# Optimization experiments

Measured on AMD Instinct MI355X. Metric: run time of the kernel, lower is better.

Reference implementation:

```python
import jax, jax.numpy as jnp
import numpy as np

N = 20000      # nodes
E = 640000     # edges
R = 90         # relations
IN_F = 128     # raw feature dim
HID = 64       # hidden_channels
OUT = 32       # out_channels of conv2
NCLASS = 4
NB = 35        # num_bases (conv1)
EPS = 1e-16    # PyG softmax epsilon


def setup_inputs() -> dict:
    key = jax.random.key(0)
    ks = jax.random.split(key, 16)
    s = 0.1
    return {
        "x": jax.random.normal(ks[0], (N, IN_F), jnp.float32),
        "edge_index": jax.random.randint(ks[1], (2, E), 0, N, jnp.int32),
        "edge_type": jax.random.randint(ks[2], (E,), 0, R, jnp.int32),
        "edge_attr": jax.random.normal(ks[3], (E, 16), jnp.float32),
        # lin1: in_channels -> hidden (no bias)
        "lin1_w": jax.random.normal(ks[4], (IN_F, HID), jnp.float32) * s,
        # conv1: basis decomposition, heads=2, out=20, dim=2 -> H*O=40, H*dim=4
        "att1": jax.random.normal(ks[5], (R, NB), jnp.float32) * s,
        "basis1": jax.random.normal(ks[6], (NB, HID, 40), jnp.float32) * s,
        "q1": jax.random.normal(ks[7], (40, 4), jnp.float32) * s,
        "k1": jax.random.normal(ks[8], (40, 4), jnp.float32) * s,
        "wmod1": jnp.ones((20,), jnp.float32),            # mod='additive' weight (init ones)
        "bias1": jnp.zeros((80,), jnp.float32),            # concat bias: H*dim*O = 80
        # conv2: block-diagonal, in=80, blocks=2, H*O=64, H*dim=2
        "w2": jax.random.normal(ks[9], (R, 2, 40, 32), jnp.float32) * s,
        "q2": jax.random.normal(ks[10], (64, 2), jnp.float32) * s,
        "k2": jax.random.normal(ks[11], (64, 2), jnp.float32) * s,
        "lin_edge_w": jax.random.normal(ks[12], (16, 64), jnp.float32) * s,
        "e2": jax.random.normal(ks[13], (64, 2), jnp.float32) * s,
        # lin2: 2*out -> nclass
        "lin2_w": jax.random.normal(ks[14], (2 * OUT, NCLASS), jnp.float32) * s,
        "lin2_b": jnp.zeros((NCLASS,), jnp.float32),
    }


def segment_softmax(alpha, seg, num_segments):
    # PyG softmax: exp(x - detach(segment_max)) / (segment_sum + 1e-16)
    m = jax.ops.segment_max(alpha, seg, num_segments=num_segments)
    e = jnp.exp(alpha - jax.lax.stop_gradient(m)[seg])
    ssum = jax.ops.segment_sum(e, seg, num_segments=num_segments)
    return e / (ssum[seg] + EPS)


def rgat_forward(x, edge_index, edge_type, edge_attr, lin1_w, att1, basis1,
                 q1, k1, wmod1, bias1, w2, q2, k2, lin_edge_w, e2, lin2_w, lin2_b):
    src, dst = edge_index[0], edge_index[1]   # x_j = x[src], x_i = x[dst]
    n = x.shape[0]
    e = src.shape[0]

    h = x @ lin1_w                            # [N, HID]

    # ---- conv1: basis decomposition, within-relation, multiplicative attn, mod='additive'
    w = jnp.einsum('rb,bio->rio', att1, basis1)          # [R, HID, 40]
    xw = jnp.einsum('ni,rio->rno', h, w)                 # [R, N, 40] (all-relation transform)
    outj = xw[edge_type, src]                            # [E, 40]
    outi = xw[edge_type, dst]                            # [E, 40]
    qi = outi @ q1                                       # [E, 4]
    kj = outj @ k1                                       # [E, 4]
    alpha = qi * kj                                      # multiplicative-self-attention
    seg = dst.astype(jnp.int32) * R + edge_type          # within-relation softmax groups
    alpha = segment_softmax(alpha, seg, n * R)           # [E, 4]
    outj4 = outj.reshape(e, 2, 1, 20)                    # [E, H, 1, O]
    hmod = wmod1 * jnp.broadcast_to(outj4, (e, 2, 2, 20))  # mod='additive' term
    msg = outj4 * alpha.reshape(e, 2, 2, 1) + hmod       # [E, H, dim, O]
    agg = jax.ops.segment_sum(msg, dst, num_segments=n)  # [N, 2, 2, 20]
    h1 = agg.reshape(n, 80) + bias1
    h1 = jax.nn.relu(h1)

    # ---- conv2: block-diagonal, across-relation, additive attn, edge features, no bias
    xb = h1.reshape(n, 2, 40)
    xw2 = jnp.einsum('nbc,rbcd->rnbd', xb, w2).reshape(R, n, 64)  # [R, N, 64]
    outj = xw2[edge_type, src]                           # [E, 64]
    outi = xw2[edge_type, dst]
    qi = outi @ q2                                       # [E, 2]
    kj = outj @ k2
    ae = (edge_attr @ lin_edge_w) @ e2                   # [E, 2]
    alpha = jax.nn.leaky_relu(qi + kj + ae, 0.2)         # additive-self-attention
    alpha = segment_softmax(alpha, dst, n)               # across-relation
    msg = alpha.reshape(e, 2, 1) * outj.reshape(e, 2, 32)
    h2 = jax.ops.segment_sum(msg, dst, num_segments=n).reshape(n, 64)

    out = h2 @ lin2_w + lin2_b
    return jax.nn.log_softmax(out, axis=-1)


def reference(x, edge_index, edge_type, edge_attr, lin1_w, att1, basis1, q1, k1,
              wmod1, bias1, w2, q2, k2, lin_edge_w, e2, lin2_w, lin2_b):
    return rgat_forward(x, edge_index, edge_type, edge_attr, lin1_w, att1, basis1,
                        q1, k1, wmod1, bias1, w2, q2, k2, lin_edge_w, e2, lin2_w, lin2_b)
```

## Files before the change

kernel.cpp:

```cpp
#include <hip/hip_runtime.h>
#include <math.h>

constexpr int NN   = 20000;
constexpr int EE   = 640000;
constexpr int RR   = 90;
constexpr int INF_ = 128;
constexpr int HID  = 64;
constexpr float EPS = 1e-16f;
constexpr int E2   = 646144;

typedef unsigned short u16;
typedef _Float16 f16;
typedef __attribute__((ext_vector_type(8))) _Float16 f16x8;
typedef __attribute__((ext_vector_type(4))) _Float16 f16x4;
typedef __attribute__((ext_vector_type(4))) float f32x4;
typedef __attribute__((ext_vector_type(4))) int ivec4;

__device__ inline unsigned f2ord(float f) {
    unsigned u = __float_as_uint(f);
    return (u & 0x80000000u) ? ~u : (u | 0x80000000u);
}
__device__ inline float ord2f(unsigned x) {
    unsigned u = (x & 0x80000000u) ? (x & 0x7FFFFFFFu) : ~x;
    return __uint_as_float(u);
}
#define ORD_NEGINF 0x007FFFFFu

__global__ void k_fillrec(int4* p, int n) {
    int i = blockIdx.x * blockDim.x + threadIdx.x;
    if (i < n) { int4 r; r.x = 0; r.y = 0; r.z = 0; r.w = -1; p[i] = r; }
}

__global__ void k_hist(const int* et, int* hist) {
    __shared__ int lh[RR];
    if (threadIdx.x < RR) lh[threadIdx.x] = 0;
    __syncthreads();
    int i = blockIdx.x * blockDim.x + threadIdx.x;
    if (i < EE) atomicAdd(&lh[et[i]], 1);
    __syncthreads();
    if (threadIdx.x < RR) atomicAdd(&hist[threadIdx.x], lh[threadIdx.x]);
}

__global__ void k_scanPad(const int* hist, int* cursor) {
    if (threadIdx.x == 0) {
        int acc = 0;
        for (int r = 0; r < RR; ++r) {
            cursor[r] = acc;
            acc += (hist[r] + 63) & ~63;
        }
    }
}

__global__ void k_scatter(const int* src, const int* dst, const int* et,
                          int* cursor, int4* sortedR, int* posS) {
    __shared__ int lh[RR];
    __shared__ int lbase[RR];
    if (threadIdx.x < RR) lh[threadIdx.x] = 0;
    __syncthreads();
    int i = blockIdx.x * blockDim.x + threadIdx.x;
    int r = et[i];
    int rank = atomicAdd(&lh[r], 1);
    __syncthreads();
    if (threadIdx.x < RR) {
        int c = lh[threadIdx.x];
        lbase[threadIdx.x] = c ? atomicAdd(&cursor[threadIdx.x], c) : 0;
    }
    __syncthreads();
    int pos = lbase[r] + rank;
    int4 rec; rec.x = src[i]; rec.y = dst[i]; rec.z = r; rec.w = i;
    sortedR[pos] = rec;
    posS[i] = pos;
}

__global__ void k_histD(const int* dst, int* histD) {
    int i = blockIdx.x * blockDim.x + threadIdx.x;
    if (i < EE) atomicAdd(&histD[dst[i]], 1);
}

__global__ void k_scanD(const int* histD, int* rowptrD, int* cursorD) {
    __shared__ int part[256];
    const int CH = (NN + 255) / 256;
    int tid = threadIdx.x;
    int base = tid * CH;
    int s = 0;
    for (int j = 0; j < CH; ++j) {
        int idx = base + j;
        if (idx < NN) s += histD[idx];
    }
    part[tid] = s;
    __syncthreads();
    if (tid == 0) {
        int acc = 0;
        for (int t = 0; t < 256; ++t) { int v = part[t]; part[t] = acc; acc += v; }
    }
    __syncthreads();
    int acc = part[tid];
    for (int j = 0; j < CH; ++j) {
        int idx = base + j;
        if (idx < NN) {
            rowptrD[idx] = acc;
            cursorD[idx] = acc;
            acc += histD[idx];
        }
    }
    if (tid == 0) rowptrD[NN] = EE;
}

__global__ void k_scatterD(int4* sortedR, int* cursorD, u16* relD) {
    int i = blockIdx.x * blockDim.x + threadIdx.x;
    if (i >= E2) return;
    int4 rec = sortedR[i];
    if (rec.w < 0) return;
    int pos = atomicAdd(&cursorD[rec.y], 1);
    ((int*)(sortedR + i))[3] = pos;
    relD[pos] = (u16)rec.z;
}

__global__ void k_w1(const float* att1, const float* basis1, float* w1) {
    int idx = blockIdx.x * blockDim.x + threadIdx.x;
    if (idx >= RR * 2560) return;
    int r = idx / 2560, co = idx - r * 2560;
    float acc = 0.f;
    for (int b = 0; b < 35; ++b) acc += att1[r * 35 + b] * basis1[b * 2560 + co];
    w1[idx] = acc;
}

__global__ void k_wqk1(const float* w1, const float* q1, const float* k1,
                       float* wq1, float* wk1) {
    int idx = blockIdx.x * blockDim.x + threadIdx.x;
    if (idx >= RR * 64 * 4) return;
    int t = idx & 3, c = (idx >> 2) & 63, r = idx >> 8;
    const float* wrow = w1 + (size_t)r * 2560 + c * 40;
    float aq = 0.f, ak = 0.f;
    for (int o = 0; o < 40; ++o) {
        float w = wrow[o];
        aq += w * q1[o * 4 + t];
        ak += w * k1[o * 4 + t];
    }
    wq1[idx] = aq; wk1[idx] = ak;
}

__global__ void k_wqk2(const float* w2, const float* q2, const float* k2,
                       float* wq2, float* wk2) {
    int idx = blockIdx.x * blockDim.x + threadIdx.x;
    if (idx >= RR * 80 * 2) return;
    int t = idx & 1, bc = (idx >> 1) % 80, r = idx / 160;
    int b = bc / 40, c = bc % 40;
    const float* wbase = w2 + (size_t)((r * 2 + b) * 40 + c) * 32;
    float aq = 0.f, ak = 0.f;
    for (int d = 0; d < 32; ++d) {
        float w = wbase[d];
        aq += w * q2[(b * 32 + d) * 2 + t];
        ak += w * k2[(b * 32 + d) * 2 + t];
    }
    wq2[idx] = aq; wk2[idx] = ak;
}

__global__ void k_we(const float* lew, const float* e2, float* we) {
    int idx = threadIdx.x;
    if (idx >= 32) return;
    int i = idx >> 1, t = idx & 1;
    float acc = 0.f;
    for (int j = 0; j < 64; ++j) acc += lew[i * 64 + j] * e2[j * 2 + t];
    we[idx] = acc;
}

__global__ __launch_bounds__(256) void k_ae(const float* ea, const float* weg,
                                            const int* posS, float* aeS) {
    __shared__ float wes[32];
    if (threadIdx.x < 32) wes[threadIdx.x] = weg[threadIdx.x];
    __syncthreads();
    int e = blockIdx.x * 256 + threadIdx.x;
    if (e >= EE) return;
    const float4* ep = (const float4*)(ea + (size_t)e * 16);
    float a0 = 0.f, a1 = 0.f;
#pragma unroll
    for (int cc = 0; cc < 4; ++cc) {
        float4 v = ep[cc];
        const float* vv = (const float*)&v;
#pragma unroll
        for (int j = 0; j < 4; ++j) {
            int ii = cc * 4 + j;
            a0 = fmaf(vv[j], wes[ii * 2 + 0], a0);
            a1 = fmaf(vv[j], wes[ii * 2 + 1], a1);
        }
    }
    float2 av; av.x = a0; av.y = a1;
    *(float2*)(aeS + (size_t)posS[e] * 2) = av;
}

__global__ void k_w1hT(const float* w1, f16* w1hT) {
    int idx = blockIdx.x * blockDim.x + threadIdx.x;
    if (idx >= RR * 48 * 64) return;
    int k = idx & 63, o = (idx >> 6) % 48, r = idx / (48 * 64);
    float v = (o < 40) ? w1[(size_t)r * 2560 + k * 40 + o] : 0.f;
    w1hT[idx] = (f16)v;
}

__global__ void k_w2hT(const float* w2, f16* w2hT) {
    int idx = blockIdx.x * blockDim.x + threadIdx.x;
    if (idx >= RR * 2 * 32 * 64) return;
    int c = idx & 63, d = (idx >> 6) & 31, b = (idx >> 11) & 1, r = idx >> 12;
    float v = (c < 40) ? w2[((((size_t)r * 2 + b) * 40) + c) * 32 + d] : 0.f;
    w2hT[idx] = (f16)v;
}

__global__ void k_h(const float* x, const float* lin1_w, f16* hh) {
    __shared__ float xs[INF_];
    int n = blockIdx.x, t = threadIdx.x;
    xs[t]      = x[(size_t)n * INF_ + t];
    xs[t + 64] = x[(size_t)n * INF_ + t + 64];
    __syncthreads();
    float acc = 0.f;
    for (int i = 0; i < INF_; ++i) acc += xs[i] * lin1_w[i * HID + t];
    hh[(size_t)n * HID + t] = (f16)acc;
}

__global__ __launch_bounds__(256) void k_c1(const int4* sortedR, const f16* hh,
                                            const f16* w1hT,
                                            const float* wq1g, const float* wk1g,
                                            float* alpha1s, f16* outj1h) {
    __shared__ float qs[256], ks[256];
    int base = blockIdx.x * 64;
    int r = sortedR[base].z;
    qs[threadIdx.x] = wq1g[(size_t)r * 256 + threadIdx.x];
    ks[threadIdx.x] = wk1g[(size_t)r * 256 + threadIdx.x];
    __syncthreads();
    int wid = threadIdx.x >> 6, l = threadIdx.x & 63;
    int e0 = base + wid * 16;
    int row16 = l & 15, g = l >> 4;
    f16x8 a[3][2];
#pragma unroll
    for (int mt = 0; mt < 3; ++mt)
#pragma unroll
        for (int kk = 0; kk < 2; ++kk)
            a[mt][kk] = *(const f16x8*)(w1hT + ((size_t)r * 48 + mt * 16 + row16) * 64 + kk * 32 + g * 8);
    ivec4 er = __builtin_nontemporal_load((const ivec4*)(sortedR + e0 + row16));
    int s = er[0], d = er[1], pd = er[3];
    f16x8 b0 = *(const f16x8*)(hh + (size_t)s * 64 + g * 8);
    f16x8 b1 = *(const f16x8*)(hh + (size_t)s * 64 + 32 + g * 8);
    f16x8 d0 = *(const f16x8*)(hh + (size_t)d * 64 + g * 8);
    f16x8 d1 = *(const f16x8*)(hh + (size_t)d * 64 + 32 + g * 8);
    float qi[4] = {0.f, 0.f, 0.f, 0.f}, kj[4] = {0.f, 0.f, 0.f, 0.f};
#pragma unroll
    for (int j = 0; j < 8; ++j) {
        int p0 = g * 8 + j, p1 = 32 + g * 8 + j;
        float dv0 = (float)d0[j], dv1 = (float)d1[j];
        float bv0 = (float)b0[j], bv1 = (float)b1[j];
#pragma unroll
        for (int t = 0; t < 4; ++t) {
            qi[t] = fmaf(dv0, qs[p0 * 4 + t], fmaf(dv1, qs[p1 * 4 + t], qi[t]));
            kj[t] = fmaf(bv0, ks[p0 * 4 + t], fmaf(bv1, ks[p1 * 4 + t], kj[t]));
        }
    }
#pragma unroll
    for (int t = 0; t < 4; ++t) {
        qi[t] += __shfl_xor(qi[t], 16); qi[t] += __shfl_xor(qi[t], 32);
        kj[t] += __shfl_xor(kj[t], 16); kj[t] += __shfl_xor(kj[t], 32);
    }
    f32x4 acc[3];
#pragma unroll
    for (int mt = 0; mt < 3; ++mt) acc[mt] = (f32x4){0.f, 0.f, 0.f, 0.f};
#pragma unroll
    for (int mt = 0; mt < 3; ++mt) {
        acc[mt] = __builtin_amdgcn_mfma_f32_16x16x32_f16(a[mt][0], b0, acc[mt], 0, 0, 0);
        acc[mt] = __builtin_amdgcn_mfma_f32_16x16x32_f16(a[mt][1], b1, acc[mt], 0, 0, 0);
    }
    if (pd < 0) return;
    if (l < 16) {
        float4 av;
        av.x = qi[0] * kj[0]; av.y = qi[1] * kj[1];
        av.z = qi[2] * kj[2]; av.w = qi[3] * kj[3];
        *(float4*)(alpha1s + (size_t)pd * 4) = av;
    }
    f16* orow = outj1h + (size_t)pd * 40;
#pragma unroll
    for (int mt = 0; mt < 3; ++mt) {
        int col = mt * 16 + g * 4;
        if (col < 40) {
            f16x4 v;
            v[0] = (f16)acc[mt][0]; v[1] = (f16)acc[mt][1];
            v[2] = (f16)acc[mt][2]; v[3] = (f16)acc[mt][3];
            *(f16x4*)(orow + col) = v;
        }
    }
}

__global__ __launch_bounds__(256) void k_aggr1(const u16* relD, const int* rowptrD,
                                               const f16* outj1h, const float* alpha1s,
                                               const float* wmod, const float* bias1,
                                               f16* h1h) {
    __shared__ unsigned smax[4][RR * 5];
    __shared__ float    ssum[4][RR * 5];
    int wid = threadIdx.x >> 6;
    int lane = threadIdx.x & 63;
    int w = blockIdx.x * 4 + wid;
    int beg = rowptrD[w], end = rowptrD[w + 1];
    unsigned* mx = smax[wid];
    float*    sm = ssum[wid];
    for (int j = beg + lane; j < end; j += 64) {
        int rb = relD[j] * 5;
        mx[rb + 0] = ORD_NEGINF; mx[rb + 1] = ORD_NEGINF;
        mx[rb + 2] = ORD_NEGINF; mx[rb + 3] = ORD_NEGINF;
        sm[rb + 0] = 0.f; sm[rb + 1] = 0.f; sm[rb + 2] = 0.f; sm[rb + 3] = 0.f;
    }
    __syncthreads();
    for (int j = beg + lane; j < end; j += 64) {
        float4 a = *(const float4*)(alpha1s + (size_t)j * 4);
        int rb = relD[j] * 5;
        atomicMax(&mx[rb + 0], f2ord(a.x));
        atomicMax(&mx[rb + 1], f2ord(a.y));
        atomicMax(&mx[rb + 2], f2ord(a.z));
        atomicMax(&mx[rb + 3], f2ord(a.w));
    }
    __syncthreads();
    for (int j = beg + lane; j < end; j += 64) {
        float4 a = *(const float4*)(alpha1s + (size_t)j * 4);
        int rb = relD[j] * 5;
        atomicAdd(&sm[rb + 0], __expf(a.x - ord2f(mx[rb + 0])));
        atomicAdd(&sm[rb + 1], __expf(a.y - ord2f(mx[rb + 1])));
        atomicAdd(&sm[rb + 2], __expf(a.z - ord2f(mx[rb + 2])));
        atomicAdd(&sm[rb + 3], __expf(a.w - ord2f(mx[rb + 3])));
    }
    __syncthreads();
    for (int t = lane; t < RR * 5; t += 64) sm[t] = 1.f / (sm[t] + EPS);
    __syncthreads();
    int hh2 = lane >= 20 ? 1 : 0;
    int oo = lane - hh2 * 20;
    float acc0 = 0.f, acc1 = 0.f, accw = 0.f;
    if (lane < 40) {
        for (int j = beg; j < end; ++j) {
            int rb = relD[j] * 5 + hh2 * 2;
            float v = (float)__builtin_nontemporal_load(outj1h + (size_t)j * 40 + lane);
            float2 a = *(const float2*)(alpha1s + (size_t)j * 4 + hh2 * 2);
            float e0 = __expf(a.x - ord2f(mx[rb]));
            float e1 = __expf(a.y - ord2f(mx[rb + 1]));
            acc0 = fmaf(v, e0 * sm[rb], acc0);
            acc1 = fmaf(v, e1 * sm[rb + 1], acc1);
            accw += v;
        }
        float wm = wmod[oo];
        int b0 = hh2 * 40 + oo;
        float o0 = fmaxf(acc0 + wm * accw + bias1[b0], 0.f);
        float o1 = fmaxf(acc1 + wm * accw + bias1[b0 + 20], 0.f);
        h1h[(size_t)w * 80 + b0]      = (f16)o0;
        h1h[(size_t)w * 80 + b0 + 20] = (f16)o1;
    }
}

__global__ __launch_bounds__(256) void k_c2(const int4* sortedR, const f16* h1h,
                                            const f16* w2hT,
                                            const float* wq2g, const float* wk2g,
                                            const float* aeS,
                                            float* alpha2s, f16* outj2h) {
    __shared__ float qs[160], ks[160];
    int base = blockIdx.x * 64;
    int r = sortedR[base].z;
    if (threadIdx.x < 160) {
        qs[threadIdx.x] = wq2g[(size_t)r * 160 + threadIdx.x];
        ks[threadIdx.x] = wk2g[(size_t)r * 160 + threadIdx.x];
    }
    __syncthreads();
    int wid = threadIdx.x >> 6, l = threadIdx.x & 63;
    int e0 = base + wid * 16;
    int row16 = l & 15, g = l >> 4;
    f16x8 a[2][2][2];
#pragma unroll
    for (int b = 0; b < 2; ++b)
#pragma unroll
        for (int mt = 0; mt < 2; ++mt)
#pragma unroll
            for (int kk = 0; kk < 2; ++kk)
                a[b][mt][kk] = *(const f16x8*)(w2hT + ((((size_t)r * 2 + b) * 32) + mt * 16 + row16) * 64 + kk * 32 + g * 8);
    ivec4 er = __builtin_nontemporal_load((const ivec4*)(sortedR + e0 + row16));
    int s = er[0], d = er[1], pd = er[3];
    f16x8 bb[2][2], dd[2][2];
#pragma unroll
    for (int b = 0; b < 2; ++b)
#pragma unroll
        for (int kk = 0; kk < 2; ++kk) {
            bb[b][kk] = *(const f16x8*)(h1h + (size_t)s * 80 + b * 40 + kk * 32 + g * 8);
            dd[b][kk] = *(const f16x8*)(h1h + (size_t)d * 80 + b * 40 + kk * 32 + g * 8);
        }
    float a0 = 0.f, a1 = 0.f;
#pragma unroll
    for (int b = 0; b < 2; ++b) {
#pragma unroll
        for (int j = 0; j < 8; ++j) {
            int p = b * 40 + g * 8 + j;
            float dv = (float)dd[b][0][j], bv = (float)bb[b][0][j];
            a0 = fmaf(dv, qs[p * 2 + 0], fmaf(bv, ks[p * 2 + 0], a0));
            a1 = fmaf(dv, qs[p * 2 + 1], fmaf(bv, ks[p * 2 + 1], a1));
        }
        if (g == 0) {
#pragma unroll
            for (int j = 0; j < 8; ++j) {
                int p = b * 40 + 32 + j;
                float dv = (float)dd[b][1][j], bv = (float)bb[b][1][j];
                a0 = fmaf(dv, qs[p * 2 + 0], fmaf(bv, ks[p * 2 + 0], a0));
                a1 = fmaf(dv, qs[p * 2 + 1], fmaf(bv, ks[p * 2 + 1], a1));
            }
        }
    }
    a0 += __shfl_xor(a0, 16); a0 += __shfl_xor(a0, 32);
    a1 += __shfl_xor(a1, 16); a1 += __shfl_xor(a1, 32);
    f32x4 acc[2][2];
#pragma unroll
    for (int b = 0; b < 2; ++b)
#pragma unroll
        for (int mt = 0; mt < 2; ++mt) acc[b][mt] = (f32x4){0.f, 0.f, 0.f, 0.f};
#pragma unroll
    for (int b = 0; b < 2; ++b)
#pragma unroll
        for (int mt = 0; mt < 2; ++mt) {
            acc[b][mt] = __builtin_amdgcn_mfma_f32_16x16x32_f16(a[b][mt][0], bb[b][0], acc[b][mt], 0, 0, 0);
            acc[b][mt] = __builtin_amdgcn_mfma_f32_16x16x32_f16(a[b][mt][1], bb[b][1], acc[b][mt], 0, 0, 0);
        }
    if (pd < 0) return;
    if (l < 16) {
        float2 aev = *(const float2*)(aeS + (size_t)(e0 + row16) * 2);
        float x0 = a0 + aev.x, x1 = a1 + aev.y;
        x0 = x0 > 0.f ? x0 : 0.2f * x0;
        x1 = x1 > 0.f ? x1 : 0.2f * x1;
        float2 av; av.x = x0; av.y = x1;
        *(float2*)(alpha2s + (size_t)pd * 2) = av;
    }
    f16* orow = outj2h + (size_t)pd * 64;
#pragma unroll
    for (int b = 0; b < 2; ++b)
#pragma unroll
        for (int mt = 0; mt < 2; ++mt) {
            f16x4 v;
            v[0] = (f16)acc[b][mt][0]; v[1] = (f16)acc[b][mt][1];
            v[2] = (f16)acc[b][mt][2]; v[3] = (f16)acc[b][mt][3];
            *(f16x4*)(orow + b * 32 + mt * 16 + g * 4) = v;
        }
}

__global__ __launch_bounds__(256) void k_aggr2(const int* rowptrD, const f16* outj2h,
                                               const float* alpha2s, float* h2) {
    int w = blockIdx.x * 4 + (threadIdx.x >> 6);
    int lane = threadIdx.x & 63;
    if (w >= NN) return;
    int beg = rowptrD[w], end = rowptrD[w + 1];
    float m0 = -INFINITY, m1 = -INFINITY;
    for (int j = beg + lane; j < end; j += 64) {
        float2 a = *(const float2*)(alpha2s + (size_t)j * 2);
        m0 = fmaxf(m0, a.x); m1 = fmaxf(m1, a.y);
    }
#pragma unroll
    for (int off = 32; off; off >>= 1) {
        m0 = fmaxf(m0, __shfl_xor(m0, off));
        m1 = fmaxf(m1, __shfl_xor(m1, off));
    }
    float s0 = 0.f, s1 = 0.f;
    for (int j = beg + lane; j < end; j += 64) {
        float2 a = *(const float2*)(alpha2s + (size_t)j * 2);
        s0 += __expf(a.x - m0); s1 += __expf(a.y - m1);
    }
#pragma unroll
    for (int off = 32; off; off >>= 1) {
        s0 += __shfl_xor(s0, off);
        s1 += __shfl_xor(s1, off);
    }
    int b = lane >> 5;
    float mb = b ? m1 : m0;
    float rs = 1.f / ((b ? s1 : s0) + EPS);
    float acc = 0.f;
    for (int j = beg; j < end; ++j) {
        float v = (float)__builtin_nontemporal_load(outj2h + (size_t)j * 64 + lane);
        float a = alpha2s[(size_t)j * 2 + b];
        acc = fmaf(v, __expf(a - mb) * rs, acc);
    }
    h2[(size_t)w * 64 + lane] = acc;
}

__global__ void k_out(const float* h2, const float* lin2_w, const float* lin2_b,
                      float* out) {
    int n = blockIdx.x * blockDim.x + threadIdx.x;
    if (n >= NN) return;
    float o[4] = {lin2_b[0], lin2_b[1], lin2_b[2], lin2_b[3]};
    const float* hr = h2 + (size_t)n * 64;
    for (int c = 0; c < 64; ++c) {
        float hv = hr[c];
#pragma unroll
        for (int t = 0; t < 4; ++t) o[t] = fmaf(hv, lin2_w[c * 4 + t], o[t]);
    }
    float m = fmaxf(fmaxf(o[0], o[1]), fmaxf(o[2], o[3]));
    float s = __expf(o[0] - m) + __expf(o[1] - m) + __expf(o[2] - m) + __expf(o[3] - m);
    float lse = m + logf(s);
#pragma unroll
    for (int t = 0; t < 4; ++t) out[(size_t)n * 4 + t] = o[t] - lse;
}

extern "C" void kernel_launch(void* const* d_in, const int* in_sizes, int n_in,
                              void* d_out, int out_size, void* d_ws, size_t ws_size,
                              hipStream_t stream) {
    const float* x        = (const float*)d_in[0];
    const int*   eidx     = (const int*)d_in[1];
    const int*   etype    = (const int*)d_in[2];
    const float* eattr    = (const float*)d_in[3];
    const float* lin1_w   = (const float*)d_in[4];
    const float* att1     = (const float*)d_in[5];
    const float* basis1   = (const float*)d_in[6];
    const float* q1       = (const float*)d_in[7];
    const float* k1       = (const float*)d_in[8];
    const float* wmod1    = (const float*)d_in[9];
    const float* bias1    = (const float*)d_in[10];
    const float* w2       = (const float*)d_in[11];
    const float* q2       = (const float*)d_in[12];
    const float* k2       = (const float*)d_in[13];
    const float* lew      = (const float*)d_in[14];
    const float* e2i      = (const float*)d_in[15];
    const float* lin2_w   = (const float*)d_in[16];
    const float* lin2_b   = (const float*)d_in[17];

    const int* src = eidx;
    const int* dst = eidx + EE;

    float* W = (float*)d_ws;
    float* w1      = W;   W += 230400;
    float* wq1     = W;   W += 23040;
    float* wk1     = W;   W += 23040;
    float* wq2     = W;   W += 14400;
    float* wk2     = W;   W += 14400;
    float* we      = W;   W += 32;
    float* h2      = W;   W += (size_t)NN * 64;
    float* aeS     = W;   W += (size_t)E2 * 2;
    f16*   hh      = (f16*)W;   W += (size_t)NN * 64 / 2;
    f16*   h1h     = (f16*)W;   W += (size_t)NN * 80 / 2 + 32;
    f16*   w1hT    = (f16*)W;   W += (size_t)RR * 48 * 64 / 2;
    f16*   w2hT    = (f16*)W;   W += (size_t)RR * 2 * 32 * 64 / 2;
    float* uni     = W;   W += (size_t)EE * 20 + (size_t)EE * 4;
    f16*   outj1h  = (f16*)uni;
    float* alpha1s = uni + (size_t)EE * 20;
    f16*   outj2h  = (f16*)uni;
    W += (size_t)EE * 8;
    float* alpha2s = W;   W += (size_t)EE * 2;
    int4*  sortedR = (int4*)W;
    int*   I = (int*)W;   I += (size_t)E2 * 4;
    u16*   relD    = (u16*)I;   I += (size_t)E2 / 2;
    int*   posS    = I;   I += EE;
    int*   rowptrD = I;   I += NN + 1;
    int*   cursorD = I;   I += NN;
    int*   histD   = I;   I += NN;
    int*   hist    = I;   I += 128;
    int*   cursor  = I;   I += 128;

    hipMemsetAsync(histD, 0, (size_t)(NN + 256) * 4, stream);
    hipMemsetAsync(h1h + (size_t)NN * 80, 0, 128, stream);
    k_fillrec<<<E2 / 256, 256, 0, stream>>>(sortedR, E2);

    k_hist<<<EE / 256, 256, 0, stream>>>(etype, hist);
    k_scanPad<<<1, 64, 0, stream>>>(hist, cursor);
    k_scatter<<<EE / 256, 256, 0, stream>>>(src, dst, etype, cursor, sortedR, posS);
    k_histD<<<EE / 256, 256, 0, stream>>>(dst, histD);
    k_scanD<<<1, 256, 0, stream>>>(histD, rowptrD, cursorD);
    k_scatterD<<<E2 / 256, 256, 0, stream>>>(sortedR, cursorD, relD);

    k_w1<<<(RR * 2560 + 255) / 256, 256, 0, stream>>>(att1, basis1, w1);
    k_wqk1<<<(RR * 256 + 255) / 256, 256, 0, stream>>>(w1, q1, k1, wq1, wk1);
    k_wqk2<<<(RR * 160 + 255) / 256, 256, 0, stream>>>(w2, q2, k2, wq2, wk2);
    k_we<<<1, 32, 0, stream>>>(lew, e2i, we);
    k_ae<<<EE / 256, 256, 0, stream>>>(eattr, we, posS, aeS);
    k_w1hT<<<(RR * 48 * 64) / 256, 256, 0, stream>>>(w1, w1hT);
    k_w2hT<<<(RR * 2 * 32 * 64) / 256, 256, 0, stream>>>(w2, w2hT);
    k_h<<<NN, 64, 0, stream>>>(x, lin1_w, hh);

    k_c1<<<E2 / 64, 256, 0, stream>>>(sortedR, hh, w1hT, wq1, wk1, alpha1s, outj1h);
    k_aggr1<<<NN / 4, 256, 0, stream>>>(relD, rowptrD, outj1h, alpha1s,
                                        wmod1, bias1, h1h);

    k_c2<<<E2 / 64, 256, 0, stream>>>(sortedR, h1h, w2hT, wq2, wk2, aeS,
                                      alpha2s, outj2h);
    k_aggr2<<<(NN + 3) / 4, 256, 0, stream>>>(rowptrD, outj2h, alpha2s, h2);

    k_out<<<(NN + 255) / 256, 256, 0, stream>>>(h2, lin2_w, lin2_b, (float*)d_out);
}
```

Baseline: 609.3 us.

## Process four edge tiles per wave with double-buffered gathers in conv kernels

In both per-edge conv kernels (k_c1, k_c2), each wave now handles 64 edges as four 16-edge tiles instead of one. It loads its own relation's q/k projections into per-wave shared memory and keeps the MFMA weight fragments in registers across all four tiles. Source and destination feature gathers are software-pipelined across two register slots, so the next tile's loads are in flight while the current tile computes. This amortises the per-relation weight loads and hides gather latency, at the cost of a quarter as many blocks and higher register pressure.

```diff
diff --git a/kernel.cpp b/kernel.cpp
--- a/kernel.cpp
+++ b/kernel.cpp
@@ -220,14 +220,17 @@
                                             const f16* w1hT,
                                             const float* wq1g, const float* wk1g,
                                             float* alpha1s, f16* outj1h) {
-    __shared__ float qs[256], ks[256];
-    int base = blockIdx.x * 64;
-    int r = sortedR[base].z;
-    qs[threadIdx.x] = wq1g[(size_t)r * 256 + threadIdx.x];
-    ks[threadIdx.x] = wk1g[(size_t)r * 256 + threadIdx.x];
-    __syncthreads();
+    __shared__ float qs[4][256], ks[4][256];
     int wid = threadIdx.x >> 6, l = threadIdx.x & 63;
-    int e0 = base + wid * 16;
+    int wbase = blockIdx.x * 256 + wid * 64;
+    int r = sortedR[wbase].z;
+    float* qw = qs[wid];
+    float* kw = ks[wid];
+    for (int t = l; t < 256; t += 64) {
+        qw[t] = wq1g[(size_t)r * 256 + t];
+        kw[t] = wk1g[(size_t)r * 256 + t];
+    }
+    __syncthreads();
     int row16 = l & 15, g = l >> 4;
     f16x8 a[3][2];
 #pragma unroll
@@ -235,55 +238,61 @@
 #pragma unroll
         for (int kk = 0; kk < 2; ++kk)
             a[mt][kk] = *(const f16x8*)(w1hT + ((size_t)r * 48 + mt * 16 + row16) * 64 + kk * 32 + g * 8);
-    ivec4 er = __builtin_nontemporal_load((const ivec4*)(sortedR + e0 + row16));
-    int s = er[0], d = er[1], pd = er[3];
-    f16x8 b0 = *(const f16x8*)(hh + (size_t)s * 64 + g * 8);
-    f16x8 b1 = *(const f16x8*)(hh + (size_t)s * 64 + 32 + g * 8);
-    f16x8 d0 = *(const f16x8*)(hh + (size_t)d * 64 + g * 8);
-    f16x8 d1 = *(const f16x8*)(hh + (size_t)d * 64 + 32 + g * 8);
-    float qi[4] = {0.f, 0.f, 0.f, 0.f}, kj[4] = {0.f, 0.f, 0.f, 0.f};
-#pragma unroll
-    for (int j = 0; j < 8; ++j) {
-        int p0 = g * 8 + j, p1 = 32 + g * 8 + j;
-        float dv0 = (float)d0[j], dv1 = (float)d1[j];
-        float bv0 = (float)b0[j], bv1 = (float)b1[j];
-#pragma unroll
-        for (int t = 0; t < 4; ++t) {
-            qi[t] = fmaf(dv0, qs[p0 * 4 + t], fmaf(dv1, qs[p1 * 4 + t], qi[t]));
-            kj[t] = fmaf(bv0, ks[p0 * 4 + t], fmaf(bv1, ks[p1 * 4 + t], kj[t]));
-        }
-    }
-#pragma unroll
-    for (int t = 0; t < 4; ++t) {
-        qi[t] += __shfl_xor(qi[t], 16); qi[t] += __shfl_xor(qi[t], 32);
-        kj[t] += __shfl_xor(kj[t], 16); kj[t] += __shfl_xor(kj[t], 32);
-    }
-    f32x4 acc[3];
-#pragma unroll
-    for (int mt = 0; mt < 3; ++mt) acc[mt] = (f32x4){0.f, 0.f, 0.f, 0.f};
-#pragma unroll
-    for (int mt = 0; mt < 3; ++mt) {
-        acc[mt] = __builtin_amdgcn_mfma_f32_16x16x32_f16(a[mt][0], b0, acc[mt], 0, 0, 0);
-        acc[mt] = __builtin_amdgcn_mfma_f32_16x16x32_f16(a[mt][1], b1, acc[mt], 0, 0, 0);
-    }
-    if (pd < 0) return;
-    if (l < 16) {
-        float4 av;
-        av.x = qi[0] * kj[0]; av.y = qi[1] * kj[1];
-        av.z = qi[2] * kj[2]; av.w = qi[3] * kj[3];
-        *(float4*)(alpha1s + (size_t)pd * 4) = av;
-    }
-    f16* orow = outj1h + (size_t)pd * 40;
-#pragma unroll
-    for (int mt = 0; mt < 3; ++mt) {
-        int col = mt * 16 + g * 4;
-        if (col < 40) {
-            f16x4 v;
-            v[0] = (f16)acc[mt][0]; v[1] = (f16)acc[mt][1];
-            v[2] = (f16)acc[mt][2]; v[3] = (f16)acc[mt][3];
-            *(f16x4*)(orow + col) = v;
-        }
-    }
+    ivec4 er[2];
+    f16x8 vb0[2], vb1[2], vd0[2], vd1[2];
+
+#define C1_LOAD(SLOT, T) { \
+    int e0_ = wbase + (T) * 16; \
+    er[SLOT] = __builtin_nontemporal_load((const ivec4*)(sortedR + e0_ + row16)); \
+    int s_ = er[SLOT][0], d_ = er[SLOT][1]; \
+    vb0[SLOT] = *(const f16x8*)(hh + (size_t)s_ * 64 + g * 8); \
+    vb1[SLOT] = *(const f16x8*)(hh + (size_t)s_ * 64 + 32 + g * 8); \
+    vd0[SLOT] = *(const f16x8*)(hh + (size_t)d_ * 64 + g * 8); \
+    vd1[SLOT] = *(const f16x8*)(hh + (size_t)d_ * 64 + 32 + g * 8); }
+
+#define C1_COMP(SLOT) { \
+    int pd_ = er[SLOT][3]; \
+    float qi[4] = {0.f,0.f,0.f,0.f}, kj[4] = {0.f,0.f,0.f,0.f}; \
+    _Pragma("unroll") for (int j = 0; j < 8; ++j) { \
+        int p0 = g * 8 + j, p1 = 32 + g * 8 + j; \
+        float dv0 = (float)vd0[SLOT][j], dv1 = (float)vd1[SLOT][j]; \
+        float bv0 = (float)vb0[SLOT][j], bv1 = (float)vb1[SLOT][j]; \
+        _Pragma("unroll") for (int t2 = 0; t2 < 4; ++t2) { \
+            qi[t2] = fmaf(dv0, qw[p0 * 4 + t2], fmaf(dv1, qw[p1 * 4 + t2], qi[t2])); \
+            kj[t2] = fmaf(bv0, kw[p0 * 4 + t2], fmaf(bv1, kw[p1 * 4 + t2], kj[t2])); } } \
+    _Pragma("unroll") for (int t2 = 0; t2 < 4; ++t2) { \
+        qi[t2] += __shfl_xor(qi[t2], 16); qi[t2] += __shfl_xor(qi[t2], 32); \
+        kj[t2] += __shfl_xor(kj[t2], 16); kj[t2] += __shfl_xor(kj[t2], 32); } \
+    f32x4 acc[3]; \
+    _Pragma("unroll") for (int mt = 0; mt < 3; ++mt) acc[mt] = (f32x4){0.f,0.f,0.f,0.f}; \
+    _Pragma("unroll") for (int mt = 0; mt < 3; ++mt) { \
+        acc[mt] = __builtin_amdgcn_mfma_f32_16x16x32_f16(a[mt][0], vb0[SLOT], acc[mt], 0, 0, 0); \
+        acc[mt] = __builtin_amdgcn_mfma_f32_16x16x32_f16(a[mt][1], vb1[SLOT], acc[mt], 0, 0, 0); } \
+    if (pd_ >= 0) { \
+        if (l < 16) { \
+            float4 av; \
+            av.x = qi[0] * kj[0]; av.y = qi[1] * kj[1]; \
+            av.z = qi[2] * kj[2]; av.w = qi[3] * kj[3]; \
+            *(float4*)(alpha1s + (size_t)pd_ * 4) = av; } \
+        f16* orow = outj1h + (size_t)pd_ * 40; \
+        _Pragma("unroll") for (int mt = 0; mt < 3; ++mt) { \
+            int col = mt * 16 + g * 4; \
+            if (col < 40) { \
+                f16x4 v; \
+                v[0] = (f16)acc[mt][0]; v[1] = (f16)acc[mt][1]; \
+                v[2] = (f16)acc[mt][2]; v[3] = (f16)acc[mt][3]; \
+                *(f16x4*)(orow + col) = v; } } } }
+
+    C1_LOAD(0, 0)
+    C1_LOAD(1, 1)
+    C1_COMP(0)
+    C1_LOAD(0, 2)
+    C1_COMP(1)
+    C1_LOAD(1, 3)
+    C1_COMP(0)
+    C1_COMP(1)
+#undef C1_LOAD
+#undef C1_COMP
 }
 
 __global__ __launch_bounds__(256) void k_aggr1(const u16* relD, const int* rowptrD,
@@ -353,16 +362,17 @@
                                             const float* wq2g, const float* wk2g,
                                             const float* aeS,
                                             float* alpha2s, f16* outj2h) {
-    __shared__ float qs[160], ks[160];
-    int base = blockIdx.x * 64;
-    int r = sortedR[base].z;
-    if (threadIdx.x < 160) {
-        qs[threadIdx.x] = wq2g[(size_t)r * 160 + threadIdx.x];
-        ks[threadIdx.x] = wk2g[(size_t)r * 160 + threadIdx.x];
-    }
-    __syncthreads();
+    __shared__ float qs[4][160], ks[4][160];
     int wid = threadIdx.x >> 6, l = threadIdx.x & 63;
-    int e0 = base + wid * 16;
+    int wbase = blockIdx.x * 256 + wid * 64;
+    int r = sortedR[wbase].z;
+    float* qw = qs[wid];
+    float* kw = ks[wid];
+    for (int t = l; t < 160; t += 64) {
+        qw[t] = wq2g[(size_t)r * 160 + t];
+        kw[t] = wk2g[(size_t)r * 160 + t];
+    }
+    __syncthreads();
     int row16 = l & 15, g = l >> 4;
     f16x8 a[2][2][2];
 #pragma unroll
@@ -372,69 +382,68 @@
 #pragma unroll
             for (int kk = 0; kk < 2; ++kk)
                 a[b][mt][kk] = *(const f16x8*)(w2hT + ((((size_t)r * 2 + b) * 32) + mt * 16 + row16) * 64 + kk * 32 + g * 8);
-    ivec4 er = __builtin_nontemporal_load((const ivec4*)(sortedR + e0 + row16));
-    int s = er[0], d = er[1], pd = er[3];
-    f16x8 bb[2][2], dd[2][2];
-#pragma unroll
-    for (int b = 0; b < 2; ++b)
-#pragma unroll
-        for (int kk = 0; kk < 2; ++kk) {
-            bb[b][kk] = *(const f16x8*)(h1h + (size_t)s * 80 + b * 40 + kk * 32 + g * 8);
-            dd[b][kk] = *(const f16x8*)(h1h + (size_t)d * 80 + b * 40 + kk * 32 + g * 8);
-        }
-    float a0 = 0.f, a1 = 0.f;
-#pragma unroll
-    for (int b = 0; b < 2; ++b) {
-#pragma unroll
-        for (int j = 0; j < 8; ++j) {
-            int p = b * 40 + g * 8 + j;
-            float dv = (float)dd[b][0][j], bv = (float)bb[b][0][j];
-            a0 = fmaf(dv, qs[p * 2 + 0], fmaf(bv, ks[p * 2 + 0], a0));
-            a1 = fmaf(dv, qs[p * 2 + 1], fmaf(bv, ks[p * 2 + 1], a1));
-        }
-        if (g == 0) {
-#pragma unroll
-            for (int j = 0; j < 8; ++j) {
-                int p = b * 40 + 32 + j;
-                float dv = (float)dd[b][1][j], bv = (float)bb[b][1][j];
-                a0 = fmaf(dv, qs[p * 2 + 0], fmaf(bv, ks[p * 2 + 0], a0));
-                a1 = fmaf(dv, qs[p * 2 + 1], fmaf(bv, ks[p * 2 + 1], a1));
-            }
-        }
-    }
-    a0 += __shfl_xor(a0, 16); a0 += __shfl_xor(a0, 32);
-    a1 += __shfl_xor(a1, 16); a1 += __shfl_xor(a1, 32);
-    f32x4 acc[2][2];
-#pragma unroll
-    for (int b = 0; b < 2; ++b)
-#pragma unroll
-        for (int mt = 0; mt < 2; ++mt) acc[b][mt] = (f32x4){0.f, 0.f, 0.f, 0.f};
-#pragma unroll
-    for (int b = 0; b < 2; ++b)
-#pragma unroll
-        for (int mt = 0; mt < 2; ++mt) {
-            acc[b][mt] = __builtin_amdgcn_mfma_f32_16x16x32_f16(a[b][mt][0], bb[b][0], acc[b][mt], 0, 0, 0);
-            acc[b][mt] = __builtin_amdgcn_mfma_f32_16x16x32_f16(a[b][mt][1], bb[b][1], acc[b][mt], 0, 0, 0);
-        }
-    if (pd < 0) return;
-    if (l < 16) {
-        float2 aev = *(const float2*)(aeS + (size_t)(e0 + row16) * 2);
-        float x0 = a0 + aev.x, x1 = a1 + aev.y;
-        x0 = x0 > 0.f ? x0 : 0.2f * x0;
-        x1 = x1 > 0.f ? x1 : 0.2f * x1;
-        float2 av; av.x = x0; av.y = x1;
-        *(float2*)(alpha2s + (size_t)pd * 2) = av;
-    }
-    f16* orow = outj2h + (size_t)pd * 64;
-#pragma unroll
-    for (int b = 0; b < 2; ++b)
-#pragma unroll
-        for (int mt = 0; mt < 2; ++mt) {
-            f16x4 v;
-            v[0] = (f16)acc[b][mt][0]; v[1] = (f16)acc[b][mt][1];
-            v[2] = (f16)acc[b][mt][2]; v[3] = (f16)acc[b][mt][3];
-            *(f16x4*)(orow + b * 32 + mt * 16 + g * 4) = v;
-        }
+    ivec4 er[2];
+    f16x8 vb[2][2][2], vd[2][2][2];
+
+#define C2_LOAD(SLOT, T) { \
+    int e0_ = wbase + (T) * 16; \
+    er[SLOT] = __builtin_nontemporal_load((const ivec4*)(sortedR + e0_ + row16)); \
+    int s_ = er[SLOT][0], d_ = er[SLOT][1]; \
+    _Pragma("unroll") for (int b = 0; b < 2; ++b) \
+        _Pragma("unroll") for (int kk = 0; kk < 2; ++kk) { \
+            vb[SLOT][b][kk] = *(const f16x8*)(h1h + (size_t)s_ * 80 + b * 40 + kk * 32 + g * 8); \
+            vd[SLOT][b][kk] = *(const f16x8*)(h1h + (size_t)d_ * 80 + b * 40 + kk * 32 + g * 8); } }
+
+#define C2_COMP(SLOT, T) { \
+    int pd_ = er[SLOT][3]; \
+    float a0 = 0.f, a1 = 0.f; \
+    _Pragma("unroll") for (int b = 0; b < 2; ++b) { \
+        _Pragma("unroll") for (int j = 0; j < 8; ++j) { \
+            int p = b * 40 + g * 8 + j; \
+            float dv = (float)vd[SLOT][b][0][j], bv = (float)vb[SLOT][b][0][j]; \
+            a0 = fmaf(dv, qw[p * 2 + 0], fmaf(bv, kw[p * 2 + 0], a0)); \
+            a1 = fmaf(dv, qw[p * 2 + 1], fmaf(bv, kw[p * 2 + 1], a1)); } \
+        if (g == 0) { \
+            _Pragma("unroll") for (int j = 0; j < 8; ++j) { \
+                int p = b * 40 + 32 + j; \
+                float dv = (float)vd[SLOT][b][1][j], bv = (float)vb[SLOT][b][1][j]; \
+                a0 = fmaf(dv, qw[p * 2 + 0], fmaf(bv, kw[p * 2 + 0], a0)); \
+                a1 = fmaf(dv, qw[p * 2 + 1], fmaf(bv, kw[p * 2 + 1], a1)); } } } \
+    a0 += __shfl_xor(a0, 16); a0 += __shfl_xor(a0, 32); \
+    a1 += __shfl_xor(a1, 16); a1 += __shfl_xor(a1, 32); \
+    f32x4 acc[2][2]; \
+    _Pragma("unroll") for (int b = 0; b < 2; ++b) \
+        _Pragma("unroll") for (int mt = 0; mt < 2; ++mt) acc[b][mt] = (f32x4){0.f,0.f,0.f,0.f}; \
+    _Pragma("unroll") for (int b = 0; b < 2; ++b) \
+        _Pragma("unroll") for (int mt = 0; mt < 2; ++mt) { \
+            acc[b][mt] = __builtin_amdgcn_mfma_f32_16x16x32_f16(a[b][mt][0], vb[SLOT][b][0], acc[b][mt], 0, 0, 0); \
+            acc[b][mt] = __builtin_amdgcn_mfma_f32_16x16x32_f16(a[b][mt][1], vb[SLOT][b][1], acc[b][mt], 0, 0, 0); } \
+    if (pd_ >= 0) { \
+        if (l < 16) { \
+            float2 aev = *(const float2*)(aeS + (size_t)(wbase + (T) * 16 + row16) * 2); \
+            float x0 = a0 + aev.x, x1 = a1 + aev.y; \
+            x0 = x0 > 0.f ? x0 : 0.2f * x0; \
+            x1 = x1 > 0.f ? x1 : 0.2f * x1; \
+            float2 av; av.x = x0; av.y = x1; \
+            *(float2*)(alpha2s + (size_t)pd_ * 2) = av; } \
+        f16* orow = outj2h + (size_t)pd_ * 64; \
+        _Pragma("unroll") for (int b = 0; b < 2; ++b) \
+            _Pragma("unroll") for (int mt = 0; mt < 2; ++mt) { \
+                f16x4 v; \
+                v[0] = (f16)acc[b][mt][0]; v[1] = (f16)acc[b][mt][1]; \
+                v[2] = (f16)acc[b][mt][2]; v[3] = (f16)acc[b][mt][3]; \
+                *(f16x4*)(orow + b * 32 + mt * 16 + g * 4) = v; } } }
+
+    C2_LOAD(0, 0)
+    C2_LOAD(1, 1)
+    C2_COMP(0, 0)
+    C2_LOAD(0, 2)
+    C2_COMP(1, 1)
+    C2_LOAD(1, 3)
+    C2_COMP(0, 2)
+    C2_COMP(1, 3)
+#undef C2_LOAD
+#undef C2_COMP
 }
 
 __global__ __launch_bounds__(256) void k_aggr2(const int* rowptrD, const f16* outj2h,
@@ -567,12 +576,12 @@
     k_w2hT<<<(RR * 2 * 32 * 64) / 256, 256, 0, stream>>>(w2, w2hT);
     k_h<<<NN, 64, 0, stream>>>(x, lin1_w, hh);
 
-    k_c1<<<E2 / 64, 256, 0, stream>>>(sortedR, hh, w1hT, wq1, wk1, alpha1s, outj1h);
+    k_c1<<<E2 / 256, 256, 0, stream>>>(sortedR, hh, w1hT, wq1, wk1, alpha1s, outj1h);
     k_aggr1<<<NN / 4, 256, 0, stream>>>(relD, rowptrD, outj1h, alpha1s,
                                         wmod1, bias1, h1h);
 
-    k_c2<<<E2 / 64, 256, 0, stream>>>(sortedR, h1h, w2hT, wq2, wk2, aeS,
-                                      alpha2s, outj2h);
+    k_c2<<<E2 / 256, 256, 0, stream>>>(sortedR, h1h, w2hT, wq2, wk2, aeS,
+                                       alpha2s, outj2h);
     k_aggr2<<<(NN + 3) / 4, 256, 0, stream>>>(rowptrD, outj2h, alpha2s, h2);
 
     k_out<<<(NN + 255) / 256, 256, 0, stream>>>(h2, lin2_w, lin2_b, (float*)d_out);
```

Measured after the change: 588.0 us. -3.5%, faster.
